# Optimization experiments

Hardware: AMD Instinct MI355X
Metric: run time of the kernel (lower is better)

Reference implementation:

```python
import jax, jax.numpy as jnp
import numpy as np

N, E, NG = 20000, 300000, 64
IN_CH, EDGE_DIM = 64, 7
H1, H2, H3 = 128, 64, 32
HEADS = 4
BN_EPS = 1e-5
NEG_SLOPE = 0.2


def _gat_params(key, in_ch, heads, out_ch, concat):
    ks = jax.random.split(key, 6)
    s_in = 1.0 / np.sqrt(in_ch)
    s_e = 1.0 / np.sqrt(EDGE_DIM)
    W = jax.random.uniform(ks[0], (in_ch, heads * out_ch), minval=-s_in, maxval=s_in)
    a_s = jax.random.uniform(ks[1], (heads, out_ch), minval=-s_in, maxval=s_in)
    a_d = jax.random.uniform(ks[2], (heads, out_ch), minval=-s_in, maxval=s_in)
    We = jax.random.uniform(ks[3], (EDGE_DIM, heads * out_ch), minval=-s_e, maxval=s_e)
    a_e = jax.random.uniform(ks[4], (heads, out_ch), minval=-s_e, maxval=s_e)
    b = jnp.zeros((heads * out_ch,) if concat else (out_ch,), jnp.float32)
    return W, a_s, a_d, We, a_e, b


def _bn_params(key, c):
    k1, k2, k3, k4 = jax.random.split(key, 4)
    g = jax.random.uniform(k1, (c,), minval=0.5, maxval=1.5)
    be = jax.random.normal(k2, (c,)) * 0.1
    rm = jax.random.normal(k3, (c,)) * 0.1
    rv = jax.random.uniform(k4, (c,), minval=0.5, maxval=1.5)
    return g, be, rm, rv


def setup_inputs() -> dict:
    key = jax.random.key(0)
    ks = jax.random.split(key, 12)
    inp = {}
    inp["x"] = jax.random.normal(ks[0], (N, IN_CH), dtype=jnp.float32)
    inp["edge_index"] = jax.random.randint(ks[1], (2, E), 0, N)
    inp["edge_attr"] = jax.random.uniform(ks[2], (E, EDGE_DIM), dtype=jnp.float32)
    inp["batch"] = jnp.sort(jax.random.randint(ks[3], (N,), 0, NG))
    inp["w1"], inp["as1"], inp["ad1"], inp["we1"], inp["ae1"], inp["b1"] = _gat_params(ks[4], IN_CH, HEADS, H1, True)
    inp["g1"], inp["bt1"], inp["rm1"], inp["rv1"] = _bn_params(ks[5], H1 * HEADS)
    inp["w2"], inp["as2"], inp["ad2"], inp["we2"], inp["ae2"], inp["b2"] = _gat_params(ks[6], H1 * HEADS, HEADS, H2, True)
    inp["g2"], inp["bt2"], inp["rm2"], inp["rv2"] = _bn_params(ks[7], H2 * HEADS)
    inp["w3"], inp["as3"], inp["ad3"], inp["we3"], inp["ae3"], inp["b3"] = _gat_params(ks[8], H2 * HEADS, 1, H3, False)
    inp["g3"], inp["bt3"], inp["rm3"], inp["rv3"] = _bn_params(ks[9], H3)
    k10a, k10b = jax.random.split(ks[10])
    s = 1.0 / np.sqrt(H3 * 2)
    inp["lw1"] = jax.random.uniform(k10a, (H3 * 2, 32), minval=-s, maxval=s)
    inp["lb1"] = jax.random.uniform(k10b, (32,), minval=-s, maxval=s)
    k11a, k11b = jax.random.split(ks[11])
    s2 = 1.0 / np.sqrt(32)
    inp["lw2"] = jax.random.uniform(k11a, (32, 1), minval=-s2, maxval=s2)
    inp["lb2"] = jax.random.uniform(k11b, (1,), minval=-s2, maxval=s2)
    return inp


def gat_conv(x, src, dst, eattr, W, a_s, a_d, We, a_e, b, heads, out_ch, concat):
    n = x.shape[0]
    # add self loops; edge_attr for loops = per-destination mean of incoming edge_attr (PyG fill_value='mean')
    deg = jax.ops.segment_sum(jnp.ones_like(eattr[:, 0]), dst, num_segments=n)
    loop_attr = jax.ops.segment_sum(eattr, dst, num_segments=n) / jnp.clip(deg, 1.0)[:, None]
    ar = jnp.arange(n)
    s = jnp.concatenate([src, ar])
    d = jnp.concatenate([dst, ar])
    ea = jnp.concatenate([eattr, loop_attr], axis=0)
    h = (x @ W).reshape(n, heads, out_ch)                       # [N,H,C]
    a_src = jnp.sum(h * a_s, axis=-1)                           # [N,H]
    a_dst = jnp.sum(h * a_d, axis=-1)
    ee = (ea @ We).reshape(-1, heads, out_ch)                   # [Etot,H,C]
    a_edge = jnp.sum(ee * a_e, axis=-1)                         # [Etot,H]
    logit = jax.nn.leaky_relu(a_src[s] + a_dst[d] + a_edge, NEG_SLOPE)
    m = jax.ops.segment_max(logit, d, num_segments=n)           # self loops => every node non-empty
    p = jnp.exp(logit - m[d])
    den = jax.ops.segment_sum(p, d, num_segments=n)
    alpha = p / den[d]                                          # [Etot,H]
    msg = (alpha[..., None] * h[s]).reshape(-1, heads * out_ch)
    out = jax.ops.segment_sum(msg, d, num_segments=n)           # [N,H*C]
    if concat:
        return out + b
    return out.reshape(n, heads, out_ch).mean(axis=1) + b


def bn_eval(x, g, be, rm, rv):
    return (x - rm) * (g / jnp.sqrt(rv + BN_EPS)) + be


def reference(x, edge_index, edge_attr, batch,
              w1, as1, ad1, we1, ae1, b1, g1, bt1, rm1, rv1,
              w2, as2, ad2, we2, ae2, b2, g2, bt2, rm2, rv2,
              w3, as3, ad3, we3, ae3, b3, g3, bt3, rm3, rv3,
              lw1, lb1, lw2, lb2):
    src, dst = edge_index[0], edge_index[1]
    h = jax.nn.relu(bn_eval(gat_conv(x, src, dst, edge_attr, w1, as1, ad1, we1, ae1, b1, HEADS, H1, True), g1, bt1, rm1, rv1))
    h = jax.nn.relu(bn_eval(gat_conv(h, src, dst, edge_attr, w2, as2, ad2, we2, ae2, b2, HEADS, H2, True), g2, bt2, rm2, rv2))
    h = jax.nn.relu(bn_eval(gat_conv(h, src, dst, edge_attr, w3, as3, ad3, we3, ae3, b3, 1, H3, False), g3, bt3, rm3, rv3))
    counts = jax.ops.segment_sum(jnp.ones_like(h[:, 0]), batch, num_segments=NG)
    mean_pool = jax.ops.segment_sum(h, batch, num_segments=NG) / jnp.clip(counts, 1.0)[:, None]
    max_pool = jax.ops.segment_max(h, batch, num_segments=NG)
    max_pool = jnp.where(counts[:, None] > 0, max_pool, 0.0)
    z = jnp.concatenate([mean_pool, max_pool], axis=1)          # [NG, 2*H3]
    z = jax.nn.relu(z @ lw1 + lb1)
    return jax.nn.sigmoid(z @ lw2 + lb2).squeeze(-1)            # [NG]
```

## Files before the change

kernel.cpp:

```cpp
#include <hip/hip_runtime.h>
#include <math.h>

#define NEG_SLOPE 0.2f
#define BN_EPS 1e-5f

typedef __attribute__((ext_vector_type(8))) short bf16x8;
typedef __attribute__((ext_vector_type(4))) float f32x4;
typedef unsigned short u16;
typedef __attribute__((ext_vector_type(4))) unsigned short u16x4;

static __device__ __forceinline__ float leaky(float v) { return v > 0.f ? v : NEG_SLOPE * v; }
static __device__ __forceinline__ float b2f(u16 b) { return __uint_as_float(((unsigned)b) << 16); }
static __device__ __forceinline__ u16 f2b(float f) {
  unsigned u = __float_as_uint(f);
  u += 0x7FFF + ((u >> 16) & 1);
  return (u16)(u >> 16);
}
static __device__ __forceinline__ float sel4(f32x4 v, int hs) {
  float a = (hs & 1) ? v[1] : v[0];
  float b = (hs & 1) ? v[3] : v[2];
  return (hs & 2) ? b : a;
}

__global__ void k_prep(const float* __restrict__ W1, const float* __restrict__ W2, const float* __restrict__ W3,
                       const float* __restrict__ AS1, const float* __restrict__ AD1,
                       const float* __restrict__ WE1, const float* __restrict__ AE1,
                       const float* __restrict__ WE2, const float* __restrict__ AE2,
                       const float* __restrict__ WE3, const float* __restrict__ AE3,
                       u16* __restrict__ Wt1, u16* __restrict__ Wt2, u16* __restrict__ Wt3,
                       float* __restrict__ ws1, float* __restrict__ wd1,
                       float* __restrict__ watt1, float* __restrict__ watt2, float* __restrict__ watt3,
                       int* __restrict__ degInt, int* __restrict__ cursor, int Nn) {
  int idx = blockIdx.x * blockDim.x + threadIdx.x;
  if (idx < 32768) {
    int k = idx >> 9, n = idx & 511;
    Wt1[n * 64 + k] = f2b(W1[idx]);
  } else if (idx < 163840) {
    int i = idx - 32768;
    int k = i >> 8, n = i & 255;
    Wt2[n * 512 + k] = f2b(W2[i]);
  } else if (idx < 172032) {
    int i = idx - 163840;
    int k = i >> 5, n = i & 31;
    Wt3[n * 256 + k] = f2b(W3[i]);
  } else if (idx < 172288) {
    int t = idx - 172032;
    int k = t >> 2, h = t & 3;
    float s1 = 0.f, s2 = 0.f;
    for (int c = 0; c < 128; c++) {
      float w = W1[k * 512 + h * 128 + c];
      s1 += w * AS1[h * 128 + c];
      s2 += w * AD1[h * 128 + c];
    }
    ws1[t] = s1; wd1[t] = s2;
  } else if (idx < 172316) {
    int t = idx - 172288;
    int d = t >> 2, h = t & 3;
    float s = 0.f;
    for (int c = 0; c < 128; c++) s += WE1[d * 512 + h * 128 + c] * AE1[h * 128 + c];
    watt1[t] = s;
  } else if (idx < 172344) {
    int t = idx - 172316;
    int d = t >> 2, h = t & 3;
    float s = 0.f;
    for (int c = 0; c < 64; c++) s += WE2[d * 256 + h * 64 + c] * AE2[h * 64 + c];
    watt2[t] = s;
  } else if (idx < 172351) {
    int d = idx - 172344;
    float s = 0.f;
    for (int c = 0; c < 32; c++) s += WE3[d * 32 + c] * AE3[c];
    watt3[d] = s;
  } else if (idx >= 172352 && idx < 172352 + Nn) {
    degInt[idx - 172352] = 0;
  } else if (idx >= 172352 + Nn && idx < 172352 + 2 * Nn) {
    cursor[idx - 172352 - Nn] = 0;
  }
}

__global__ void k_deg(const int* __restrict__ dst, int* __restrict__ degInt, int E) {
  int e = blockIdx.x * blockDim.x + threadIdx.x;
  if (e < E) atomicAdd(&degInt[dst[e]], 1);
}

__global__ void k_scan(const int* __restrict__ degInt, int* __restrict__ rowStart, int n) {
  __shared__ int sums[1024];
  int tid = threadIdx.x;
  int per = (n + 1023) / 1024;
  int start = tid * per;
  int end = start + per; if (end > n) end = n;
  int s = 0;
  for (int i = start; i < end; i++) s += degInt[i];
  sums[tid] = s;
  __syncthreads();
  for (int off = 1; off < 1024; off <<= 1) {
    int v = (tid >= off) ? sums[tid - off] : 0;
    __syncthreads();
    sums[tid] += v;
    __syncthreads();
  }
  int base = (tid > 0) ? sums[tid - 1] : 0;
  for (int i = start; i < end; i++) { rowStart[i] = base; base += degInt[i]; }
  if (tid == 1023) rowStart[n] = sums[1023];
}

__global__ void k_fill_csr_ae(const int* __restrict__ src, const int* __restrict__ dst,
                              const float* __restrict__ eattr,
                              const int* __restrict__ rowStart, int* __restrict__ cursor,
                              int* __restrict__ csrSrc,
                              const float* __restrict__ watt1, const float* __restrict__ watt2,
                              const float* __restrict__ watt3,
                              float* __restrict__ ae1, float* __restrict__ ae2,
                              float* __restrict__ ae3, int E) {
  int e = blockIdx.x * blockDim.x + threadIdx.x;
  if (e >= E) return;
  int d = dst[e];
  int pos = rowStart[d] + atomicAdd(&cursor[d], 1);
  csrSrc[pos] = src[e];
  float ea[7];
#pragma unroll
  for (int dd = 0; dd < 7; dd++) ea[dd] = eattr[e * 7 + dd];
  f32x4 o1, o2;
#pragma unroll
  for (int h = 0; h < 4; h++) {
    float a1 = 0.f, a2 = 0.f;
#pragma unroll
    for (int dd = 0; dd < 7; dd++) { a1 += ea[dd] * watt1[dd * 4 + h]; a2 += ea[dd] * watt2[dd * 4 + h]; }
    o1[h] = a1; o2[h] = a2;
  }
  float a3 = 0.f;
#pragma unroll
  for (int dd = 0; dd < 7; dd++) a3 += ea[dd] * watt3[dd];
  *(f32x4*)(ae1 + (size_t)pos * 4) = o1;
  *(f32x4*)(ae2 + (size_t)pos * 4) = o2;
  ae3[pos] = a3;
}

__global__ __launch_bounds__(256) void k_cast_attn_x(const float* __restrict__ x, u16* __restrict__ xbf,
                                                     const float* __restrict__ ws, const float* __restrict__ wd,
                                                     float* __restrict__ asrc, float* __restrict__ adst, int Nn) {
  int n = blockIdx.x * 4 + (threadIdx.x >> 6);
  if (n >= Nn) return;
  int lane = threadIdx.x & 63;
  float xv = x[(size_t)n * 64 + lane];
  xbf[(size_t)n * 64 + lane] = f2b(xv);
  f32x4 vs = *(const f32x4*)(ws + lane * 4);
  f32x4 vd = *(const f32x4*)(wd + lane * 4);
  f32x4 s1, s2;
#pragma unroll
  for (int h = 0; h < 4; h++) { s1[h] = xv * vs[h]; s2[h] = xv * vd[h]; }
#pragma unroll
  for (int off = 1; off < 64; off <<= 1) {
#pragma unroll
    for (int h = 0; h < 4; h++) { s1[h] += __shfl_xor(s1[h], off); s2[h] += __shfl_xor(s2[h], off); }
  }
  if (lane == 0) {
    *(f32x4*)(asrc + n * 4) = s1;
    *(f32x4*)(adst + n * 4) = s2;
  }
}

template <int BM, int BN, int WM, int WN, bool EPI, int ATTN_H>
__global__ __launch_bounds__(256) void k_gemm_mfma(const u16* __restrict__ A,
                                                   const u16* __restrict__ Bt,
                                                   u16* __restrict__ Cout,
                                                   int M, int K, int Nc, int lda, int ldc,
                                                   int AzOff, int BzOff, int CzOff,
                                                   const float* __restrict__ bias,
                                                   const float* __restrict__ bng,
                                                   const float* __restrict__ bnb,
                                                   const float* __restrict__ bnrm,
                                                   const float* __restrict__ bnrv,
                                                   const float* __restrict__ a_s,
                                                   const float* __restrict__ a_d,
                                                   float* __restrict__ asrc,
                                                   float* __restrict__ adst) {
  constexpr int BK = 64;
  constexpr int LDT = BK + 8;
  __shared__ u16 As[BM][LDT];
  __shared__ u16 Bs[BN][LDT];
  constexpr int NWN = BN / WN;
  constexpr int M_REP = WM / 16;
  constexpr int N_REP = WN / 16;
  int z = blockIdx.z;
  A += (size_t)z * AzOff;
  Bt += (size_t)z * BzOff;
  Cout += (size_t)z * CzOff;
  if (EPI) {
    bias += (size_t)z * CzOff; bng += (size_t)z * CzOff; bnb += (size_t)z * CzOff;
    bnrm += (size_t)z * CzOff; bnrv += (size_t)z * CzOff;
  }
  int tid = threadIdx.x;
  int wid = tid >> 6, lane = tid & 63;
  int wr = wid / NWN, wc = wid % NWN;
  int bm = blockIdx.x * BM, bn = blockIdx.y * BN;
  int l15 = lane & 15, l4 = lane >> 4;

  f32x4 acc[M_REP][N_REP];
#pragma unroll
  for (int m = 0; m < M_REP; m++)
#pragma unroll
    for (int n = 0; n < N_REP; n++) acc[m][n] = (f32x4){0.f, 0.f, 0.f, 0.f};

  for (int k0 = 0; k0 < K; k0 += BK) {
    constexpr int CHA = BM * BK / 8;
#pragma unroll
    for (int ch0 = 0; ch0 < CHA; ch0 += 256) {
      int ch = ch0 + tid;
      int row = ch >> 3, cc = (ch & 7) * 8;
      int gr = bm + row;
      bf16x8 v = {};
      if (gr < M) v = *(const bf16x8*)(A + (size_t)gr * lda + k0 + cc);
      *(bf16x8*)(&As[row][cc]) = v;
    }
    constexpr int CHB = BN * BK / 8;
#pragma unroll
    for (int ch0 = 0; ch0 < CHB; ch0 += 256) {
      int ch = ch0 + tid;
      int row = ch >> 3, cc = (ch & 7) * 8;
      int gr = bn + row;
      bf16x8 v = {};
      if (gr < Nc) v = *(const bf16x8*)(Bt + (size_t)gr * K + k0 + cc);
      *(bf16x8*)(&Bs[row][cc]) = v;
    }
    __syncthreads();
#pragma unroll
    for (int ks = 0; ks < BK; ks += 32) {
      bf16x8 af[M_REP], bfr[N_REP];
#pragma unroll
      for (int m = 0; m < M_REP; m++)
        af[m] = *(const bf16x8*)(&As[wr * WM + m * 16 + l15][ks + l4 * 8]);
#pragma unroll
      for (int n = 0; n < N_REP; n++)
        bfr[n] = *(const bf16x8*)(&Bs[wc * WN + n * 16 + l15][ks + l4 * 8]);
#pragma unroll
      for (int m = 0; m < M_REP; m++)
#pragma unroll
        for (int n = 0; n < N_REP; n++)
          acc[m][n] = __builtin_amdgcn_mfma_f32_16x16x32_bf16(af[m], bfr[n], acc[m][n], 0, 0, 0);
    }
    __syncthreads();
  }
#pragma unroll
  for (int m = 0; m < M_REP; m++) {
#pragma unroll
    for (int r = 0; r < 4; r++) {
      int grow = bm + wr * WM + m * 16 + l4 * 4 + r;
      if (grow >= M) continue;
#pragma unroll
      for (int n = 0; n < N_REP; n++) {
        int gcol = bn + wc * WN + n * 16 + l15;
        if (gcol >= Nc) continue;
        float v = acc[m][n][r];
        if (EPI) {
          v += bias[gcol];
          v = (v - bnrm[gcol]) * (bng[gcol] * rsqrtf(bnrv[gcol] + BN_EPS)) + bnb[gcol];
          v = fmaxf(v, 0.f);
        }
        Cout[(size_t)grow * ldc + gcol] = f2b(v);
      }
    }
  }
  if (ATTN_H > 0) {
    int h = blockIdx.y * NWN + wc;
#pragma unroll
    for (int m = 0; m < M_REP; m++) {
#pragma unroll
      for (int r = 0; r < 4; r++) {
        float s1 = 0.f, s2 = 0.f;
#pragma unroll
        for (int n = 0; n < N_REP; n++) {
          float av = acc[m][n][r];
          int cc = n * 16 + l15;
          s1 += av * a_s[h * WN + cc];
          s2 += av * a_d[h * WN + cc];
        }
#pragma unroll
        for (int off = 1; off < 16; off <<= 1) { s1 += __shfl_xor(s1, off); s2 += __shfl_xor(s2, off); }
        int grow = bm + wr * WM + m * 16 + l4 * 4 + r;
        if (l15 == 0 && grow < M) {
          asrc[grow * ATTN_H + h] = s1;
          adst[grow * ATTN_H + h] = s2;
        }
      }
    }
  }
}

__global__ __launch_bounds__(256) void k_gather_x(
    const int* __restrict__ rowStart, const int* __restrict__ csrSrc,
    const float* __restrict__ aeC, const float* __restrict__ asrc, const float* __restrict__ adst,
    const u16* __restrict__ xbf, u16* __restrict__ aggOut, int Nn) {
  int wid = threadIdx.x >> 6;
  int n = blockIdx.x * 4 + wid;
  if (n >= Nn) return;
  int lane = threadIdx.x & 63;
  __shared__ float pbuf[4][64 * 4];
  int r0 = rowStart[n], r1 = rowStart[n + 1];
  f32x4 vaN = *(const f32x4*)(asrc + n * 4);
  f32x4 vdN = *(const f32x4*)(adst + n * 4);

  f32x4 m = {-1e30f, -1e30f, -1e30f, -1e30f};
  f32x4 denl = {0.f, 0.f, 0.f, 0.f};
  f32x4 aes = {0.f, 0.f, 0.f, 0.f};
  f32x4 acc = {0.f, 0.f, 0.f, 0.f};

  const f32x4* AE4 = (const f32x4*)aeC;
  for (int base = r0; base < r1; base += 64) {
    int slot = base + lane;
    bool valid = slot < r1;
    int srcl = 0;
    f32x4 lg = {-1e30f, -1e30f, -1e30f, -1e30f};
    if (valid) {
      srcl = csrSrc[slot];
      f32x4 vaS = *(const f32x4*)(asrc + srcl * 4);
      f32x4 ae = AE4[slot];
#pragma unroll
      for (int h = 0; h < 4; h++) { aes[h] += ae[h]; lg[h] = leaky(vaS[h] + vdN[h] + ae[h]); }
    }
    f32x4 mc = lg;
#pragma unroll
    for (int off = 1; off < 64; off <<= 1) {
#pragma unroll
      for (int h = 0; h < 4; h++) mc[h] = fmaxf(mc[h], __shfl_xor(mc[h], off));
    }
    f32x4 rr;
#pragma unroll
    for (int h = 0; h < 4; h++) {
      float mn = fmaxf(m[h], mc[h]);
      rr[h] = __expf(m[h] - mn);
      m[h] = mn;
      denl[h] *= rr[h];
      acc[h] *= rr[h];
    }
    f32x4 ex;
#pragma unroll
    for (int h = 0; h < 4; h++) ex[h] = valid ? __expf(lg[h] - m[h]) : 0.f;
#pragma unroll
    for (int h = 0; h < 4; h++) denl[h] += ex[h];
    *(f32x4*)(&pbuf[wid][lane * 4]) = ex;
    int nv = r1 - base; if (nv > 64) nv = 64;
    int j = 0;
    for (; j + 3 < nv; j += 4) {
      int s0 = __shfl(srcl, j);
      int s1 = __shfl(srcl, j + 1);
      int s2 = __shfl(srcl, j + 2);
      int s3 = __shfl(srcl, j + 3);
      f32x4 p0 = *(const f32x4*)(&pbuf[wid][j * 4]);
      f32x4 p1 = *(const f32x4*)(&pbuf[wid][(j + 1) * 4]);
      f32x4 p2 = *(const f32x4*)(&pbuf[wid][(j + 2) * 4]);
      f32x4 p3 = *(const f32x4*)(&pbuf[wid][(j + 3) * 4]);
      float x0 = b2f(xbf[(size_t)s0 * 64 + lane]);
      float x1 = b2f(xbf[(size_t)s1 * 64 + lane]);
      float x2 = b2f(xbf[(size_t)s2 * 64 + lane]);
      float x3 = b2f(xbf[(size_t)s3 * 64 + lane]);
#pragma unroll
      for (int h = 0; h < 4; h++)
        acc[h] += p0[h] * x0 + p1[h] * x1 + p2[h] * x2 + p3[h] * x3;
    }
    for (; j < nv; j++) {
      int s0 = __shfl(srcl, j);
      f32x4 p0 = *(const f32x4*)(&pbuf[wid][j * 4]);
      float x0 = b2f(xbf[(size_t)s0 * 64 + lane]);
#pragma unroll
      for (int h = 0; h < 4; h++) acc[h] += p0[h] * x0;
    }
  }
  float degf = fmaxf((float)(r1 - r0), 1.0f);
  f32x4 ls, exs;
#pragma unroll
  for (int h = 0; h < 4; h++) {
    float a = aes[h];
#pragma unroll
    for (int off = 1; off < 64; off <<= 1) a += __shfl_xor(a, off);
    ls[h] = leaky(vaN[h] + vdN[h] + a / degf);
    float mn = fmaxf(m[h], ls[h]);
    float sc = __expf(m[h] - mn);
    m[h] = mn;
    denl[h] *= sc;
    acc[h] *= sc;
    exs[h] = __expf(ls[h] - mn);
  }
  f32x4 den;
#pragma unroll
  for (int h = 0; h < 4; h++) {
    float v = denl[h];
#pragma unroll
    for (int off = 1; off < 64; off <<= 1) v += __shfl_xor(v, off);
    den[h] = v + exs[h];
  }
  {
    float xn = b2f(xbf[(size_t)n * 64 + lane]);
#pragma unroll
    for (int h = 0; h < 4; h++) acc[h] += exs[h] * xn;
  }
#pragma unroll
  for (int h = 0; h < 4; h++) pbuf[wid][h * 64 + lane] = acc[h] / den[h];
  u16x4 ov;
#pragma unroll
  for (int jj = 0; jj < 4; jj++) ov[jj] = f2b(pbuf[wid][lane * 4 + jj]);
  *(u16x4*)(aggOut + (size_t)n * 256 + lane * 4) = ov;
}

template <int C, int CPL>
__global__ __launch_bounds__(256) void k_gather4(
    const int* __restrict__ rowStart, const int* __restrict__ csrSrc,
    const float* __restrict__ aeC, const float* __restrict__ asrc, const float* __restrict__ adst,
    const u16* __restrict__ hbuf, const float* __restrict__ bias,
    const float* __restrict__ bng, const float* __restrict__ bnb,
    const float* __restrict__ bnrm, const float* __restrict__ bnrv,
    u16* __restrict__ outbuf, int Nn) {
  constexpr int HC = 4 * C;
  typedef __attribute__((ext_vector_type(CPL))) unsigned short u16v;
  int wid = threadIdx.x >> 6;
  int n = blockIdx.x * 4 + wid;
  if (n >= Nn) return;
  int lane = threadIdx.x & 63;
  int hs = lane >> 4;
  __shared__ float pbuf[4][64 * 4];
  int r0 = rowStart[n], r1 = rowStart[n + 1];
  f32x4 vaN = *(const f32x4*)(asrc + n * 4);
  f32x4 vdN = *(const f32x4*)(adst + n * 4);

  f32x4 m = {-1e30f, -1e30f, -1e30f, -1e30f};
  f32x4 denl = {0.f, 0.f, 0.f, 0.f};
  f32x4 aes = {0.f, 0.f, 0.f, 0.f};
  float acc[CPL];
#pragma unroll
  for (int jj = 0; jj < CPL; jj++) acc[jj] = 0.f;

  const f32x4* AE4 = (const f32x4*)aeC;
  for (int base = r0; base < r1; base += 64) {
    int slot = base + lane;
    bool valid = slot < r1;
    int srcl = 0;
    f32x4 lg = {-1e30f, -1e30f, -1e30f, -1e30f};
    if (valid) {
      srcl = csrSrc[slot];
      f32x4 vaS = *(const f32x4*)(asrc + srcl * 4);
      f32x4 ae = AE4[slot];
#pragma unroll
      for (int h = 0; h < 4; h++) { aes[h] += ae[h]; lg[h] = leaky(vaS[h] + vdN[h] + ae[h]); }
    }
    f32x4 mc = lg;
#pragma unroll
    for (int off = 1; off < 64; off <<= 1) {
#pragma unroll
      for (int h = 0; h < 4; h++) mc[h] = fmaxf(mc[h], __shfl_xor(mc[h], off));
    }
    f32x4 rr;
#pragma unroll
    for (int h = 0; h < 4; h++) {
      float mn = fmaxf(m[h], mc[h]);
      rr[h] = __expf(m[h] - mn);
      m[h] = mn;
      denl[h] *= rr[h];
    }
    float rrh = sel4(rr, hs);
#pragma unroll
    for (int jj = 0; jj < CPL; jj++) acc[jj] *= rrh;
    f32x4 ex;
#pragma unroll
    for (int h = 0; h < 4; h++) ex[h] = valid ? __expf(lg[h] - m[h]) : 0.f;
#pragma unroll
    for (int h = 0; h < 4; h++) denl[h] += ex[h];
    *(f32x4*)(&pbuf[wid][lane * 4]) = ex;
    int nv = r1 - base; if (nv > 64) nv = 64;
    int j = 0;
    for (; j + 3 < nv; j += 4) {
      int s0 = __shfl(srcl, j);
      int s1 = __shfl(srcl, j + 1);
      int s2 = __shfl(srcl, j + 2);
      int s3 = __shfl(srcl, j + 3);
      float p0 = pbuf[wid][j * 4 + hs];
      float p1 = pbuf[wid][(j + 1) * 4 + hs];
      float p2 = pbuf[wid][(j + 2) * 4 + hs];
      float p3 = pbuf[wid][(j + 3) * 4 + hs];
      u16v h0 = *(const u16v*)(hbuf + (size_t)s0 * HC + lane * CPL);
      u16v h1 = *(const u16v*)(hbuf + (size_t)s1 * HC + lane * CPL);
      u16v h2 = *(const u16v*)(hbuf + (size_t)s2 * HC + lane * CPL);
      u16v h3 = *(const u16v*)(hbuf + (size_t)s3 * HC + lane * CPL);
#pragma unroll
      for (int jj = 0; jj < CPL; jj++)
        acc[jj] += p0 * b2f(h0[jj]) + p1 * b2f(h1[jj]) + p2 * b2f(h2[jj]) + p3 * b2f(h3[jj]);
    }
    for (; j < nv; j++) {
      int s0 = __shfl(srcl, j);
      float p0 = pbuf[wid][j * 4 + hs];
      u16v h0 = *(const u16v*)(hbuf + (size_t)s0 * HC + lane * CPL);
#pragma unroll
      for (int jj = 0; jj < CPL; jj++) acc[jj] += p0 * b2f(h0[jj]);
    }
  }
  float degf = fmaxf((float)(r1 - r0), 1.0f);
  f32x4 ls, exs, scv;
#pragma unroll
  for (int h = 0; h < 4; h++) {
    float a = aes[h];
#pragma unroll
    for (int off = 1; off < 64; off <<= 1) a += __shfl_xor(a, off);
    ls[h] = leaky(vaN[h] + vdN[h] + a / degf);
    float mn = fmaxf(m[h], ls[h]);
    scv[h] = __expf(m[h] - mn);
    m[h] = mn;
    denl[h] *= scv[h];
    exs[h] = __expf(ls[h] - mn);
  }
  float sch = sel4(scv, hs);
#pragma unroll
  for (int jj = 0; jj < CPL; jj++) acc[jj] *= sch;
  f32x4 den;
#pragma unroll
  for (int h = 0; h < 4; h++) {
    float v = denl[h];
#pragma unroll
    for (int off = 1; off < 64; off <<= 1) v += __shfl_xor(v, off);
    den[h] = v + exs[h];
  }
  {
    float ps = sel4(exs, hs);
    u16v hN = *(const u16v*)(hbuf + (size_t)n * HC + lane * CPL);
#pragma unroll
    for (int jj = 0; jj < CPL; jj++) acc[jj] += ps * b2f(hN[jj]);
  }
  float dh = sel4(den, hs);
  u16v ov;
#pragma unroll
  for (int jj = 0; jj < CPL; jj++) {
    int c = lane * CPL + jj;
    float v = acc[jj] / dh + bias[c];
    v = (v - bnrm[c]) * (bng[c] * rsqrtf(bnrv[c] + BN_EPS)) + bnb[c];
    ov[jj] = f2b(fmaxf(v, 0.f));
  }
  *(u16v*)(outbuf + (size_t)n * HC + lane * CPL) = ov;
}

__global__ __launch_bounds__(256) void k_gather_L3(
    const int* __restrict__ rowStart, const int* __restrict__ csrSrc,
    const float* __restrict__ ae3, const float* __restrict__ asrc, const float* __restrict__ adst,
    const u16* __restrict__ hbuf, const float* __restrict__ bias,
    const float* __restrict__ bng, const float* __restrict__ bnb,
    const float* __restrict__ bnrm, const float* __restrict__ bnrv,
    u16* __restrict__ outbuf, int Nn) {
  int wid = threadIdx.x >> 6;
  int n = blockIdx.x * 4 + wid;
  if (n >= Nn) return;
  int lane = threadIdx.x & 63;
  int cl = lane & 31, half = lane >> 5;
  __shared__ float pbuf[4][64];
  int r0 = rowStart[n], r1 = rowStart[n + 1];
  float vaN = asrc[n], vdN = adst[n];

  float m = -1e30f, denl = 0.f, aes = 0.f, acc = 0.f;
  for (int base = r0; base < r1; base += 64) {
    int slot = base + lane;
    bool valid = slot < r1;
    int srcl = 0;
    float lg = -1e30f;
    if (valid) {
      srcl = csrSrc[slot];
      float ae = ae3[slot];
      aes += ae;
      lg = leaky(asrc[srcl] + vdN + ae);
    }
    float mc = lg;
#pragma unroll
    for (int off = 1; off < 64; off <<= 1) mc = fmaxf(mc, __shfl_xor(mc, off));
    float mn = fmaxf(m, mc);
    float sc = __expf(m - mn);
    m = mn;
    denl *= sc;
    acc *= sc;
    float ex = valid ? __expf(lg - m) : 0.f;
    denl += ex;
    pbuf[wid][lane] = ex;
    int nv = r1 - base; if (nv > 64) nv = 64;
    for (int j = half; j < nv; j += 2) {
      float p = pbuf[wid][j];
      int s = __shfl(srcl, j);
      acc += p * b2f(hbuf[(size_t)s * 32 + cl]);
    }
  }
#pragma unroll
  for (int off = 1; off < 64; off <<= 1) aes += __shfl_xor(aes, off);
  float degf = fmaxf((float)(r1 - r0), 1.0f);
  float ls = leaky(vaN + vdN + aes / degf);
  float mn = fmaxf(m, ls);
  float sc = __expf(m - mn);
  denl *= sc;
  acc *= sc;
  float exs = __expf(ls - mn);
#pragma unroll
  for (int off = 1; off < 64; off <<= 1) denl += __shfl_xor(denl, off);
  float den = denl + exs;
  if (half == 0) acc += exs * b2f(hbuf[(size_t)n * 32 + cl]);
  acc += __shfl_xor(acc, 32);
  if (half == 0) {
    float v = acc / den + bias[cl];
    v = (v - bnrm[cl]) * (bng[cl] * rsqrtf(bnrv[cl] + BN_EPS)) + bnb[cl];
    outbuf[(size_t)n * 32 + cl] = f2b(fmaxf(v, 0.f));
  }
}

__global__ __launch_bounds__(256) void k_pool_mlp(
    const u16* __restrict__ h3, const int* __restrict__ batch, int Nn,
    const float* __restrict__ lw1, const float* __restrict__ lb1,
    const float* __restrict__ lw2, const float* __restrict__ lb2,
    float* __restrict__ out) {
  int g = blockIdx.x;
  int tid = threadIdx.x;
  __shared__ int s_lo, s_hi;
  if (tid == 0) {
    int lo = 0, hi = Nn;
    while (lo < hi) { int mid = (lo + hi) >> 1; if (batch[mid] < g) lo = mid + 1; else hi = mid; }
    s_lo = lo;
    int lo2 = lo, hi2 = Nn;
    while (lo2 < hi2) { int mid = (lo2 + hi2) >> 1; if (batch[mid] < g + 1) lo2 = mid + 1; else hi2 = mid; }
    s_hi = lo2;
  }
  __syncthreads();
  int lo = s_lo, hi = s_hi;
  int c = tid & 31, r = tid >> 5;
  float sum = 0.f, mx = -1e30f;
  for (int n = lo + r; n < hi; n += 8) {
    float v = b2f(h3[(size_t)n * 32 + c]);
    sum += v;
    mx = fmaxf(mx, v);
  }
  __shared__ float ssum[8][32];
  __shared__ float smax[8][32];
  ssum[r][c] = sum;
  smax[r][c] = mx;
  __syncthreads();
  __shared__ float z[64];
  __shared__ float zz1[32];
  if (tid < 32) {
    float s = 0.f, m2 = -1e30f;
#pragma unroll
    for (int rr = 0; rr < 8; rr++) { s += ssum[rr][tid]; m2 = fmaxf(m2, smax[rr][tid]); }
    int cnt = hi - lo;
    z[tid] = s / fmaxf((float)cnt, 1.0f);
    z[32 + tid] = (cnt > 0) ? m2 : 0.f;
  }
  __syncthreads();
  if (tid < 32) {
    float s = lb1[tid];
    for (int k = 0; k < 64; k++) s += z[k] * lw1[k * 32 + tid];
    zz1[tid] = fmaxf(s, 0.f);
  }
  __syncthreads();
  if (tid == 0) {
    float s = lb2[0];
    for (int j = 0; j < 32; j++) s += zz1[j] * lw2[j];
    out[g] = 1.f / (1.f + expf(-s));
  }
}

extern "C" void kernel_launch(void* const* d_in, const int* in_sizes, int n_in,
                              void* d_out, int out_size, void* d_ws, size_t ws_size,
                              hipStream_t stream) {
  const float* x     = (const float*)d_in[0];
  const int*   eidx  = (const int*)d_in[1];
  const float* eattr = (const float*)d_in[2];
  const int*   batch = (const int*)d_in[3];
  int N = in_sizes[0] / 64;
  int E = in_sizes[1] / 2;
  int NG = out_size;
  const int* src = eidx;
  const int* dst = eidx + E;

  const float* W[3]  = {(const float*)d_in[4],  (const float*)d_in[14], (const float*)d_in[24]};
  const float* AS[3] = {(const float*)d_in[5],  (const float*)d_in[15], (const float*)d_in[25]};
  const float* AD[3] = {(const float*)d_in[6],  (const float*)d_in[16], (const float*)d_in[26]};
  const float* WE[3] = {(const float*)d_in[7],  (const float*)d_in[17], (const float*)d_in[27]};
  const float* AE[3] = {(const float*)d_in[8],  (const float*)d_in[18], (const float*)d_in[28]};
  const float* B[3]  = {(const float*)d_in[9],  (const float*)d_in[19], (const float*)d_in[29]};
  const float* G[3]  = {(const float*)d_in[10], (const float*)d_in[20], (const float*)d_in[30]};
  const float* BT[3] = {(const float*)d_in[11], (const float*)d_in[21], (const float*)d_in[31]};
  const float* RM[3] = {(const float*)d_in[12], (const float*)d_in[22], (const float*)d_in[32]};
  const float* RV[3] = {(const float*)d_in[13], (const float*)d_in[23], (const float*)d_in[33]};
  const float* lw1 = (const float*)d_in[34];
  const float* lb1 = (const float*)d_in[35];
  const float* lw2 = (const float*)d_in[36];
  const float* lb2 = (const float*)d_in[37];

  char* wp = (char*)d_ws;
  auto alloc = [&](size_t bytes) -> void* {
    void* p = (void*)wp;
    wp += (bytes + 255) & ~(size_t)255;
    return p;
  };
  u16*   xbf      = (u16*)alloc((size_t)N * 64 * 2);
  u16*   aggB     = (u16*)alloc((size_t)N * 256 * 2);
  u16*   bufH     = (u16*)alloc((size_t)N * 512 * 2);
  u16*   bufA     = (u16*)alloc((size_t)N * 512 * 2);
  u16*   Wt1      = (u16*)alloc((size_t)512 * 64 * 2);
  u16*   Wt2      = (u16*)alloc((size_t)256 * 512 * 2);
  u16*   Wt3      = (u16*)alloc((size_t)32 * 256 * 2);
  int*   degInt   = (int*)alloc((size_t)N * 4);
  int*   cursor   = (int*)alloc((size_t)N * 4);
  int*   rowStart = (int*)alloc((size_t)(N + 1) * 4);
  int*   csrSrc   = (int*)alloc((size_t)E * 4);
  float* ae1      = (float*)alloc((size_t)E * 4 * 4);
  float* ae2      = (float*)alloc((size_t)E * 4 * 4);
  float* ae3buf   = (float*)alloc((size_t)E * 4);
  float* asrc     = (float*)alloc((size_t)N * 4 * 4);
  float* adst     = (float*)alloc((size_t)N * 4 * 4);
  float* watt1    = (float*)alloc(28 * 4);
  float* watt2    = (float*)alloc(28 * 4);
  float* watt3    = (float*)alloc(7 * 4);
  float* ws1      = (float*)alloc(64 * 4 * 4);
  float* wd1      = (float*)alloc(64 * 4 * 4);

  int prepTotal = 172352 + 2 * N;
  k_prep<<<(prepTotal + 255) / 256, 256, 0, stream>>>(
      W[0], W[1], W[2], AS[0], AD[0], WE[0], AE[0], WE[1], AE[1], WE[2], AE[2],
      Wt1, Wt2, Wt3, ws1, wd1, watt1, watt2, watt3, degInt, cursor, N);

  k_deg<<<(E + 255) / 256, 256, 0, stream>>>(dst, degInt, E);
  k_scan<<<1, 1024, 0, stream>>>(degInt, rowStart, N);
  k_fill_csr_ae<<<(E + 255) / 256, 256, 0, stream>>>(src, dst, eattr, rowStart, cursor, csrSrc,
                                                     watt1, watt2, watt3, ae1, ae2, ae3buf, E);

  int gmM = (N + 127) / 128;
  int nb4 = (N + 3) / 4;

  k_cast_attn_x<<<nb4, 256, 0, stream>>>(x, xbf, ws1, wd1, asrc, adst, N);
  k_gather_x<<<nb4, 256, 0, stream>>>(rowStart, csrSrc, ae1, asrc, adst, xbf, aggB, N);
  k_gemm_mfma<128, 128, 64, 64, true, 0><<<dim3(gmM, 1, 4), 256, 0, stream>>>(
      aggB, Wt1, bufA, N, 64, 128, 256, 512, 64, 128 * 64, 128,
      B[0], G[0], BT[0], RM[0], RV[0], nullptr, nullptr, nullptr, nullptr);

  k_gemm_mfma<128, 128, 64, 64, false, 4><<<dim3(gmM, 2, 1), 256, 0, stream>>>(
      bufA, Wt2, bufH, N, 512, 256, 512, 256, 0, 0, 0,
      nullptr, nullptr, nullptr, nullptr, nullptr, AS[1], AD[1], asrc, adst);
  k_gather4<64, 4><<<nb4, 256, 0, stream>>>(rowStart, csrSrc, ae2, asrc, adst,
                                            bufH, B[1], G[1], BT[1], RM[1], RV[1], bufA, N);

  k_gemm_mfma<128, 32, 32, 32, false, 1><<<dim3(gmM, 1, 1), 256, 0, stream>>>(
      bufA, Wt3, bufH, N, 256, 32, 256, 32, 0, 0, 0,
      nullptr, nullptr, nullptr, nullptr, nullptr, AS[2], AD[2], asrc, adst);
  k_gather_L3<<<nb4, 256, 0, stream>>>(rowStart, csrSrc, ae3buf, asrc, adst,
                                       bufH, B[2], G[2], BT[2], RM[2], RV[2], bufA, N);

  k_pool_mlp<<<NG, 256, 0, stream>>>(bufA, batch, N, lw1, lb1, lw2, lb2, (float*)d_out);
}
```

Measured before the change: 256.6 us.

## Fuse prep, degree count and x cast into one launch; unroll gathers by eight

```diff
diff --git a/kernel.cpp b/kernel.cpp
--- a/kernel.cpp
+++ b/kernel.cpp
@@ -22,64 +22,172 @@
   return (hs & 2) ? b : a;
 }
 
-__global__ void k_prep(const float* __restrict__ W1, const float* __restrict__ W2, const float* __restrict__ W3,
-                       const float* __restrict__ AS1, const float* __restrict__ AD1,
-                       const float* __restrict__ WE1, const float* __restrict__ AE1,
-                       const float* __restrict__ WE2, const float* __restrict__ AE2,
-                       const float* __restrict__ WE3, const float* __restrict__ AE3,
-                       u16* __restrict__ Wt1, u16* __restrict__ Wt2, u16* __restrict__ Wt3,
-                       float* __restrict__ ws1, float* __restrict__ wd1,
-                       float* __restrict__ watt1, float* __restrict__ watt2, float* __restrict__ watt3,
-                       int* __restrict__ degInt, int* __restrict__ cursor, int Nn) {
-  int idx = blockIdx.x * blockDim.x + threadIdx.x;
-  if (idx < 32768) {
-    int k = idx >> 9, n = idx & 511;
-    Wt1[n * 64 + k] = f2b(W1[idx]);
-  } else if (idx < 163840) {
-    int i = idx - 32768;
-    int k = i >> 8, n = i & 255;
-    Wt2[n * 512 + k] = f2b(W2[i]);
-  } else if (idx < 172032) {
-    int i = idx - 163840;
-    int k = i >> 5, n = i & 31;
-    Wt3[n * 256 + k] = f2b(W3[i]);
-  } else if (idx < 172288) {
-    int t = idx - 172032;
-    int k = t >> 2, h = t & 3;
-    float s1 = 0.f, s2 = 0.f;
-    for (int c = 0; c < 128; c++) {
-      float w = W1[k * 512 + h * 128 + c];
-      s1 += w * AS1[h * 128 + c];
-      s2 += w * AD1[h * 128 + c];
-    }
-    ws1[t] = s1; wd1[t] = s2;
-  } else if (idx < 172316) {
-    int t = idx - 172288;
-    int d = t >> 2, h = t & 3;
-    float s = 0.f;
-    for (int c = 0; c < 128; c++) s += WE1[d * 512 + h * 128 + c] * AE1[h * 128 + c];
-    watt1[t] = s;
-  } else if (idx < 172344) {
-    int t = idx - 172316;
-    int d = t >> 2, h = t & 3;
-    float s = 0.f;
-    for (int c = 0; c < 64; c++) s += WE2[d * 256 + h * 64 + c] * AE2[h * 64 + c];
-    watt2[t] = s;
-  } else if (idx < 172351) {
-    int d = idx - 172344;
-    float s = 0.f;
-    for (int c = 0; c < 32; c++) s += WE3[d * 32 + c] * AE3[c];
-    watt3[d] = s;
-  } else if (idx >= 172352 && idx < 172352 + Nn) {
-    degInt[idx - 172352] = 0;
-  } else if (idx >= 172352 + Nn && idx < 172352 + 2 * Nn) {
-    cursor[idx - 172352 - Nn] = 0;
-  }
-}
-
-__global__ void k_deg(const int* __restrict__ dst, int* __restrict__ degInt, int E) {
-  int e = blockIdx.x * blockDim.x + threadIdx.x;
-  if (e < E) atomicAdd(&degInt[dst[e]], 1);
+#define PREP_ITEMS 172352
+#define PREP_BLOCKS 674
+
+__global__ __launch_bounds__(256) void k_mega(
+    const float* __restrict__ W1, const float* __restrict__ W2, const float* __restrict__ W3,
+    const float* __restrict__ AS1, const float* __restrict__ AD1,
+    const float* __restrict__ WE1, const float* __restrict__ AE1,
+    const float* __restrict__ WE2, const float* __restrict__ AE2,
+    const float* __restrict__ WE3, const float* __restrict__ AE3,
+    u16* __restrict__ Wt1, u16* __restrict__ Wt2, u16* __restrict__ Wt3,
+    float* __restrict__ ws1, float* __restrict__ wd1,
+    float* __restrict__ watt1, float* __restrict__ watt2, float* __restrict__ watt3,
+    const int* __restrict__ dst, int* __restrict__ degInt, int E, int degB,
+    const float* __restrict__ x, u16* __restrict__ xbf,
+    float* __restrict__ asrc, float* __restrict__ adst, int Nn) {
+  int bid = blockIdx.x;
+  int tid = threadIdx.x;
+  if (bid < PREP_BLOCKS) {
+    int idx = bid * 256 + tid;
+    if (idx < 32768) {
+      int k = idx >> 9, n = idx & 511;
+      Wt1[n * 64 + k] = f2b(W1[idx]);
+    } else if (idx < 163840) {
+      int i = idx - 32768;
+      int k = i >> 8, n = i & 255;
+      Wt2[n * 512 + k] = f2b(W2[i]);
+    } else if (idx < 172032) {
+      int i = idx - 163840;
+      int k = i >> 5, n = i & 31;
+      Wt3[n * 256 + k] = f2b(W3[i]);
+    } else if (idx < 172288) {
+      int t = idx - 172032;
+      int k = t >> 2, h = t & 3;
+      float s1 = 0.f, s2 = 0.f;
+      for (int c = 0; c < 128; c++) {
+        float w = W1[k * 512 + h * 128 + c];
+        s1 += w * AS1[h * 128 + c];
+        s2 += w * AD1[h * 128 + c];
+      }
+      ws1[t] = s1; wd1[t] = s2;
+    } else if (idx < 172316) {
+      int t = idx - 172288;
+      int d = t >> 2, h = t & 3;
+      float s = 0.f;
+      for (int c = 0; c < 128; c++) s += WE1[d * 512 + h * 128 + c] * AE1[h * 128 + c];
+      watt1[t] = s;
+    } else if (idx < 172344) {
+      int t = idx - 172316;
+      int d = t >> 2, h = t & 3;
+      float s = 0.f;
+      for (int c = 0; c < 64; c++) s += WE2[d * 256 + h * 64 + c] * AE2[h * 64 + c];
+      watt2[t] = s;
+    } else if (idx < 172351) {
+      int d = idx - 172344;
+      float s = 0.f;
+      for (int c = 0; c < 32; c++) s += WE3[d * 32 + c] * AE3[c];
+      watt3[d] = s;
+    }
+  } else if (bid < PREP_BLOCKS + degB) {
+    int e = (bid - PREP_BLOCKS) * 256 + tid;
+    if (e < E) atomicAdd(&degInt[dst[e]], 1);
+  } else {
+    int n = (bid - PREP_BLOCKS - degB) * 4 + (tid >> 6);
+    if (n >= Nn) return;
+    int lane = tid & 63;
+    float xv = x[(size_t)n * 64 + lane];
+    xbf[(size_t)n * 64 + lane] = f2b(xv);
+    f32x4 vs = *(const f32x4*)(ws1 + lane * 4);
+    f32x4 vd = *(const f32x4*)(wd1 + lane * 4);
+    f32x4 s1, s2;
+#pragma unroll
+    for (int h = 0; h < 4; h++) { s1[h] = xv * vs[h]; s2[h] = xv * vd[h]; }
+#pragma unroll
+    for (int off = 1; off < 64; off <<= 1) {
+#pragma unroll
+      for (int h = 0; h < 4; h++) { s1[h] += __shfl_xor(s1[h], off); s2[h] += __shfl_xor(s2[h], off); }
+    }
+    if (lane == 0) {
+      *(f32x4*)(asrc + n * 4) = s1;
+      *(f32x4*)(adst + n * 4) = s2;
+    }
+  }
+}
+
+
+__global__ __launch_bounds__(256) void k_mega2(
+    const float* __restrict__ W1, const float* __restrict__ W2, const float* __restrict__ W3,
+    const float* __restrict__ AS1, const float* __restrict__ AD1,
+    const float* __restrict__ WE1, const float* __restrict__ AE1,
+    const float* __restrict__ WE2, const float* __restrict__ AE2,
+    const float* __restrict__ WE3, const float* __restrict__ AE3,
+    u16* __restrict__ Wt1, u16* __restrict__ Wt2, u16* __restrict__ Wt3,
+    float* __restrict__ watt1, float* __restrict__ watt2, float* __restrict__ watt3,
+    const int* __restrict__ dst, int* __restrict__ degInt, int E, int degB,
+    const float* __restrict__ x, u16* __restrict__ xbf,
+    float* __restrict__ asrc, float* __restrict__ adst, int Nn) {
+  int bid = blockIdx.x;
+  int tid = threadIdx.x;
+  if (bid < PREP_BLOCKS) {
+    int idx = bid * 256 + tid;
+    if (idx < 32768) {
+      int k = idx >> 9, n = idx & 511;
+      Wt1[n * 64 + k] = f2b(W1[idx]);
+    } else if (idx < 163840) {
+      int i = idx - 32768;
+      int k = i >> 8, n = i & 255;
+      Wt2[n * 512 + k] = f2b(W2[i]);
+    } else if (idx < 172032) {
+      int i = idx - 163840;
+      int k = i >> 5, n = i & 31;
+      Wt3[n * 256 + k] = f2b(W3[i]);
+    } else if (idx < 172060) {
+      int t = idx - 172032;
+      int d = t >> 2, h = t & 3;
+      float s = 0.f;
+      for (int c = 0; c < 128; c++) s += WE1[d * 512 + h * 128 + c] * AE1[h * 128 + c];
+      watt1[t] = s;
+    } else if (idx < 172088) {
+      int t = idx - 172060;
+      int d = t >> 2, h = t & 3;
+      float s = 0.f;
+      for (int c = 0; c < 64; c++) s += WE2[d * 256 + h * 64 + c] * AE2[h * 64 + c];
+      watt2[t] = s;
+    } else if (idx < 172095) {
+      int d = idx - 172088;
+      float s = 0.f;
+      for (int c = 0; c < 32; c++) s += WE3[d * 32 + c] * AE3[c];
+      watt3[d] = s;
+    }
+  } else if (bid < PREP_BLOCKS + degB) {
+    int e = (bid - PREP_BLOCKS) * 256 + tid;
+    if (e < E) atomicAdd(&degInt[dst[e]], 1);
+  } else {
+    __shared__ float lws[256], lwd[256];
+    {
+      int t = tid;
+      int k = t >> 2, h = t & 3;
+      float s1 = 0.f, s2 = 0.f;
+      for (int c = 0; c < 128; c++) {
+        float w = W1[k * 512 + h * 128 + c];
+        s1 += w * AS1[h * 128 + c];
+        s2 += w * AD1[h * 128 + c];
+      }
+      lws[t] = s1; lwd[t] = s2;
+    }
+    __syncthreads();
+    int n = (bid - PREP_BLOCKS - degB) * 4 + (tid >> 6);
+    if (n >= Nn) return;
+    int lane = tid & 63;
+    float xv = x[(size_t)n * 64 + lane];
+    xbf[(size_t)n * 64 + lane] = f2b(xv);
+    f32x4 vs = *(const f32x4*)(lws + lane * 4);
+    f32x4 vd = *(const f32x4*)(lwd + lane * 4);
+    f32x4 s1, s2;
+#pragma unroll
+    for (int h = 0; h < 4; h++) { s1[h] = xv * vs[h]; s2[h] = xv * vd[h]; }
+#pragma unroll
+    for (int off = 1; off < 64; off <<= 1) {
+#pragma unroll
+      for (int h = 0; h < 4; h++) { s1[h] += __shfl_xor(s1[h], off); s2[h] += __shfl_xor(s2[h], off); }
+    }
+    if (lane == 0) {
+      *(f32x4*)(asrc + n * 4) = s1;
+      *(f32x4*)(adst + n * 4) = s2;
+    }
+  }
 }
 
 __global__ void k_scan(const int* __restrict__ degInt, int* __restrict__ rowStart, int n) {
@@ -133,30 +241,6 @@
   *(f32x4*)(ae1 + (size_t)pos * 4) = o1;
   *(f32x4*)(ae2 + (size_t)pos * 4) = o2;
   ae3[pos] = a3;
-}
-
-__global__ __launch_bounds__(256) void k_cast_attn_x(const float* __restrict__ x, u16* __restrict__ xbf,
-                                                     const float* __restrict__ ws, const float* __restrict__ wd,
-                                                     float* __restrict__ asrc, float* __restrict__ adst, int Nn) {
-  int n = blockIdx.x * 4 + (threadIdx.x >> 6);
-  if (n >= Nn) return;
-  int lane = threadIdx.x & 63;
-  float xv = x[(size_t)n * 64 + lane];
-  xbf[(size_t)n * 64 + lane] = f2b(xv);
-  f32x4 vs = *(const f32x4*)(ws + lane * 4);
-  f32x4 vd = *(const f32x4*)(wd + lane * 4);
-  f32x4 s1, s2;
-#pragma unroll
-  for (int h = 0; h < 4; h++) { s1[h] = xv * vs[h]; s2[h] = xv * vd[h]; }
-#pragma unroll
-  for (int off = 1; off < 64; off <<= 1) {
-#pragma unroll
-    for (int h = 0; h < 4; h++) { s1[h] += __shfl_xor(s1[h], off); s2[h] += __shfl_xor(s2[h], off); }
-  }
-  if (lane == 0) {
-    *(f32x4*)(asrc + n * 4) = s1;
-    *(f32x4*)(adst + n * 4) = s2;
-  }
 }
 
 template <int BM, int BN, int WM, int WN, bool EPI, int ATTN_H>
@@ -340,22 +424,19 @@
     *(f32x4*)(&pbuf[wid][lane * 4]) = ex;
     int nv = r1 - base; if (nv > 64) nv = 64;
     int j = 0;
-    for (; j + 3 < nv; j += 4) {
-      int s0 = __shfl(srcl, j);
-      int s1 = __shfl(srcl, j + 1);
-      int s2 = __shfl(srcl, j + 2);
-      int s3 = __shfl(srcl, j + 3);
-      f32x4 p0 = *(const f32x4*)(&pbuf[wid][j * 4]);
-      f32x4 p1 = *(const f32x4*)(&pbuf[wid][(j + 1) * 4]);
-      f32x4 p2 = *(const f32x4*)(&pbuf[wid][(j + 2) * 4]);
-      f32x4 p3 = *(const f32x4*)(&pbuf[wid][(j + 3) * 4]);
-      float x0 = b2f(xbf[(size_t)s0 * 64 + lane]);
-      float x1 = b2f(xbf[(size_t)s1 * 64 + lane]);
-      float x2 = b2f(xbf[(size_t)s2 * 64 + lane]);
-      float x3 = b2f(xbf[(size_t)s3 * 64 + lane]);
-#pragma unroll
-      for (int h = 0; h < 4; h++)
-        acc[h] += p0[h] * x0 + p1[h] * x1 + p2[h] * x2 + p3[h] * x3;
+    for (; j + 7 < nv; j += 8) {
+      int ss[8];
+      float xs[8];
+#pragma unroll
+      for (int q = 0; q < 8; q++) ss[q] = __shfl(srcl, j + q);
+#pragma unroll
+      for (int q = 0; q < 8; q++) xs[q] = b2f(xbf[(size_t)ss[q] * 64 + lane]);
+#pragma unroll
+      for (int q = 0; q < 8; q++) {
+        f32x4 p = *(const f32x4*)(&pbuf[wid][(j + q) * 4]);
+#pragma unroll
+        for (int h = 0; h < 4; h++) acc[h] += p[h] * xs[q];
+      }
     }
     for (; j < nv; j++) {
       int s0 = __shfl(srcl, j);
@@ -466,22 +547,19 @@
     *(f32x4*)(&pbuf[wid][lane * 4]) = ex;
     int nv = r1 - base; if (nv > 64) nv = 64;
     int j = 0;
-    for (; j + 3 < nv; j += 4) {
-      int s0 = __shfl(srcl, j);
-      int s1 = __shfl(srcl, j + 1);
-      int s2 = __shfl(srcl, j + 2);
-      int s3 = __shfl(srcl, j + 3);
-      float p0 = pbuf[wid][j * 4 + hs];
-      float p1 = pbuf[wid][(j + 1) * 4 + hs];
-      float p2 = pbuf[wid][(j + 2) * 4 + hs];
-      float p3 = pbuf[wid][(j + 3) * 4 + hs];
-      u16v h0 = *(const u16v*)(hbuf + (size_t)s0 * HC + lane * CPL);
-      u16v h1 = *(const u16v*)(hbuf + (size_t)s1 * HC + lane * CPL);
-      u16v h2 = *(const u16v*)(hbuf + (size_t)s2 * HC + lane * CPL);
-      u16v h3 = *(const u16v*)(hbuf + (size_t)s3 * HC + lane * CPL);
-#pragma unroll
-      for (int jj = 0; jj < CPL; jj++)
-        acc[jj] += p0 * b2f(h0[jj]) + p1 * b2f(h1[jj]) + p2 * b2f(h2[jj]) + p3 * b2f(h3[jj]);
+    for (; j + 7 < nv; j += 8) {
+      int ss[8];
+#pragma unroll
+      for (int q = 0; q < 8; q++) ss[q] = __shfl(srcl, j + q);
+      u16v hv[8];
+#pragma unroll
+      for (int q = 0; q < 8; q++) hv[q] = *(const u16v*)(hbuf + (size_t)ss[q] * HC + lane * CPL);
+#pragma unroll
+      for (int q = 0; q < 8; q++) {
+        float p = pbuf[wid][(j + q) * 4 + hs];
+#pragma unroll
+        for (int jj = 0; jj < CPL; jj++) acc[jj] += p * b2f(hv[q][jj]);
+      }
     }
     for (; j < nv; j++) {
       int s0 = __shfl(srcl, j);
@@ -708,23 +786,25 @@
   float* watt1    = (float*)alloc(28 * 4);
   float* watt2    = (float*)alloc(28 * 4);
   float* watt3    = (float*)alloc(7 * 4);
-  float* ws1      = (float*)alloc(64 * 4 * 4);
-  float* wd1      = (float*)alloc(64 * 4 * 4);
-
-  int prepTotal = 172352 + 2 * N;
-  k_prep<<<(prepTotal + 255) / 256, 256, 0, stream>>>(
+
+  size_t zspan = (size_t)((char*)cursor - (char*)degInt) + (size_t)N * 4;
+  hipMemsetAsync(degInt, 0, zspan, stream);
+
+  int degB = (E + 255) / 256;
+  int nb4 = (N + 3) / 4;
+  int megaBlocks = PREP_BLOCKS + degB + nb4;
+
+  k_mega2<<<megaBlocks, 256, 0, stream>>>(
       W[0], W[1], W[2], AS[0], AD[0], WE[0], AE[0], WE[1], AE[1], WE[2], AE[2],
-      Wt1, Wt2, Wt3, ws1, wd1, watt1, watt2, watt3, degInt, cursor, N);
-
-  k_deg<<<(E + 255) / 256, 256, 0, stream>>>(dst, degInt, E);
+      Wt1, Wt2, Wt3, watt1, watt2, watt3,
+      dst, degInt, E, degB, x, xbf, asrc, adst, N);
+
   k_scan<<<1, 1024, 0, stream>>>(degInt, rowStart, N);
   k_fill_csr_ae<<<(E + 255) / 256, 256, 0, stream>>>(src, dst, eattr, rowStart, cursor, csrSrc,
                                                      watt1, watt2, watt3, ae1, ae2, ae3buf, E);
 
   int gmM = (N + 127) / 128;
-  int nb4 = (N + 3) / 4;
-
-  k_cast_attn_x<<<nb4, 256, 0, stream>>>(x, xbf, ws1, wd1, asrc, adst, N);
+
   k_gather_x<<<nb4, 256, 0, stream>>>(rowStart, csrSrc, ae1, asrc, adst, xbf, aggB, N);
   k_gemm_mfma<128, 128, 64, 64, true, 0><<<dim3(gmM, 1, 4), 256, 0, stream>>>(
       aggB, Wt1, bufA, N, 64, 128, 256, 512, 64, 128 * 64, 128,
```

New measurement: 452.0 us. +76.1%, slower.
